# Kernel optimization log

Measured on AMD Instinct MI355X. Metric: run time of the kernel, lower is better.

## Reference

```python
import jax, jax.numpy as jnp
import numpy as np

N_HEADS = 16
ATT_DIM = 1024
HEAD_DIM = ATT_DIM // N_HEADS
SCALE = 1.0 / (HEAD_DIM ** 0.5)


def setup_inputs() -> dict:
    key = jax.random.key(0)
    k1, k2 = jax.random.split(key)
    B, N, D = 4, 2048, 1024
    X = jax.random.normal(k1, (B, N, D), dtype=jnp.float32)
    W_qkv = jax.random.normal(k2, (3 * ATT_DIM, D), dtype=jnp.float32) * 0.02  # trunc_normal-ish std
    return {"X": X, "W_qkv": W_qkv}


def reference(X, W_qkv):
    B, N, D = X.shape
    # qkv projection (bias=False): X @ W^T -> [b, n, 3*att_dim]
    QKV = jnp.einsum('bnd,od->bno', X, W_qkv)
    # rearrange 'b n (p h d) -> p b h n d'
    QKV = QKV.reshape(B, N, 3, N_HEADS, HEAD_DIM).transpose(2, 0, 3, 1, 4)
    Q, K, V = QKV[0], QKV[1], QKV[2]
    # scaled dot-product attention, full NxN scores (as in source)
    scores = jnp.einsum('bhid,bhjd->bhij', Q, K) * SCALE
    S = jax.nn.softmax(scores, axis=-1)
    # dropout rate is 0.0 -> identity
    Y = jnp.einsum('bhij,bhjd->bhid', S, V)
    # 'b h n d -> b n (h d)'; out_proj is Identity (out_dim == att_dim)
    return Y.transpose(0, 2, 1, 3).reshape(B, N, N_HEADS * HEAD_DIM)
```

## Files before the change

### kernel.cpp

```cpp
#include <hip/hip_runtime.h>

#define BATCH   4
#define SEQ     2048
#define DMODEL  1024
#define NHEADS  16
#define HDIM    64
#define QSC     0.18033688f

typedef short s16x8 __attribute__((ext_vector_type(8)));
typedef float f32x4 __attribute__((ext_vector_type(4)));
typedef const __attribute__((address_space(1))) unsigned int* gas_t;
typedef __attribute__((address_space(3))) unsigned int* las_t;

__device__ inline unsigned short f2bf(float f) {
    unsigned int u = __float_as_uint(f);
    u += 0x7FFF + ((u >> 16) & 1);
    return (unsigned short)(u >> 16);
}

__device__ __forceinline__ float exp2_fast(float x) {
#if __has_builtin(__builtin_amdgcn_exp2f)
    return __builtin_amdgcn_exp2f(x);
#else
    return exp2f(x);
#endif
}

__device__ __forceinline__ float rcp_fast(float x) {
#if __has_builtin(__builtin_amdgcn_rcpf)
    return __builtin_amdgcn_rcpf(x);
#else
    return 1.0f / x;
#endif
}

__device__ __forceinline__ unsigned int pack_bf16x2(float lo, float hi) {
    unsigned int a = __float_as_uint(lo) + 0x8000u;
    unsigned int b = __float_as_uint(hi) + 0x8000u;
#if __has_builtin(__builtin_amdgcn_perm)
    return __builtin_amdgcn_perm(b, a, 0x07060302u);
#else
    return (a >> 16) | (b & 0xFFFF0000u);
#endif
}

__global__ void cvt_bf16_2(const float* __restrict__ a,
                           unsigned short* __restrict__ oa, int n4a,
                           const float* __restrict__ bsrc,
                           unsigned short* __restrict__ ob, int n4b) {
    int i = blockIdx.x * blockDim.x + threadIdx.x;
    if (i < n4a) {
        float4 v = ((const float4*)a)[i];
        ushort4 o;
        o.x = f2bf(v.x); o.y = f2bf(v.y); o.z = f2bf(v.z); o.w = f2bf(v.w);
        ((ushort4*)oa)[i] = o;
    } else {
        int j = i - n4a;
        if (j < n4b) {
            float4 v = ((const float4*)bsrc)[j];
            ushort4 o;
            o.x = f2bf(v.x); o.y = f2bf(v.y); o.z = f2bf(v.z); o.w = f2bf(v.w);
            ((ushort4*)ob)[j] = o;
        }
    }
}

__global__ __launch_bounds__(256) void qkv_gemm(
    const unsigned short* __restrict__ Xb,
    const unsigned short* __restrict__ Wb,
    unsigned short* __restrict__ Qo,
    unsigned short* __restrict__ Ko,
    unsigned short* __restrict__ Vt)
{
    __shared__ __align__(16) unsigned short As[2 * 128 * 32];
    __shared__ __align__(16) unsigned short Bs[2 * 128 * 32];

    const int t    = threadIdx.x;
    const int flat = blockIdx.y * 24 + blockIdx.x;
    const int sw   = (flat & 7) * 192 + (flat >> 3);
    const int m0   = (sw / 24) * 128;
    const int n0   = (sw % 24) * 128;

    const int wid  = t >> 6;
    const int lane = t & 63;
    const int l15  = lane & 15;
    const int quad = lane >> 4;
    const int wm   = (wid >> 1) * 64;
    const int wn   = (wid & 1) * 64;

    const int rA   = wid * 32 + (lane >> 2);
    const int kcol_phys = (lane & 3) * 8;
    const int kcol_src  = ((lane & 3) ^ ((rA >> 1) & 3)) * 8;
    const unsigned short* gA = &Xb[(size_t)(m0 + rA) * 1024 + kcol_src];
    const unsigned short* gB = &Wb[(size_t)(n0 + rA) * 1024 + kcol_src];

    const int cswq = (quad ^ ((l15 >> 1) & 3)) * 8;

    f32x4 acc[4][4] = {};

    auto stage = [&](int k0, int bufE) {
        #pragma unroll
        for (int rd = 0; rd < 2; rd++) {
            __builtin_amdgcn_global_load_lds(
                (gas_t)(const void*)(gA + rd * 16 * 1024 + k0),
                (las_t)(void*)&As[bufE + (rA + rd * 16) * 32 + kcol_phys], 16, 0, 0);
            __builtin_amdgcn_global_load_lds(
                (gas_t)(const void*)(gB + rd * 16 * 1024 + k0),
                (las_t)(void*)&Bs[bufE + (rA + rd * 16) * 32 + kcol_phys], 16, 0, 0);
        }
    };

    auto comp = [&](int bufE) {
        s16x8 af[4], bf[4];
        #pragma unroll
        for (int mt = 0; mt < 4; mt++)
            af[mt] = *(const s16x8*)&As[bufE + (wm + mt * 16 + l15) * 32 + cswq];
        #pragma unroll
        for (int nt = 0; nt < 4; nt++)
            bf[nt] = *(const s16x8*)&Bs[bufE + (wn + nt * 16 + l15) * 32 + cswq];
        #pragma unroll
        for (int mt = 0; mt < 4; mt++)
            #pragma unroll
            for (int nt = 0; nt < 4; nt++)
                acc[mt][nt] = __builtin_amdgcn_mfma_f32_16x16x32_bf16(
                    af[mt], bf[nt], acc[mt][nt], 0, 0, 0);
    };

    stage(0, 0);
    __syncthreads();

    #pragma unroll 1
    for (int k0 = 0; k0 < 1024; k0 += 64) {
        stage(k0 + 32, 4096);
        comp(0);
        __syncthreads();
        if (k0 + 64 < 1024) stage(k0 + 64, 0);
        comp(4096);
        __syncthreads();
    }

    #pragma unroll
    for (int mt = 0; mt < 4; mt++) {
        const int mbase = m0 + wm + mt * 16 + quad * 4;
        const int b     = mbase >> 11;
        const int nbase = mbase & 2047;
        #pragma unroll
        for (int nt = 0; nt < 4; nt++) {
            const int o  = n0 + wn + nt * 16 + l15;
            const int p  = o >> 10;
            const int oo = o & 1023;
            const int h  = oo >> 6;
            const int d  = oo & 63;
            if (p == 0) {
                #pragma unroll
                for (int r = 0; r < 4; r++)
                    Qo[((size_t)(b * 16 + h) * 2048 + nbase + r) * 64 + d] =
                        f2bf(acc[mt][nt][r] * QSC);
            } else if (p == 1) {
                #pragma unroll
                for (int r = 0; r < 4; r++)
                    Ko[((size_t)(b * 16 + h) * 2048 + nbase + r) * 64 + d] =
                        f2bf(acc[mt][nt][r]);
            } else {
                ushort4 v4;
                v4.x = f2bf(acc[mt][nt][0]);
                v4.y = f2bf(acc[mt][nt][1]);
                v4.z = f2bf(acc[mt][nt][2]);
                v4.w = f2bf(acc[mt][nt][3]);
                *(ushort4*)&Vt[((size_t)(b * 16 + h) * 64 + d) * 2048 + nbase] = v4;
            }
        }
    }
}

#define PSTRIDE 72
#define PBASE   16384

__global__ __launch_bounds__(512) void attn(
    const unsigned short* __restrict__ Q,
    const unsigned short* __restrict__ K,
    const unsigned short* __restrict__ Vt,
    float* __restrict__ out)
{
    __shared__ __align__(16) unsigned short LDS[PBASE + 8 * 32 * PSTRIDE];

    const int t    = threadIdx.x;
    const int w    = t >> 6;
    const int lane = t & 63;
    const int l15  = lane & 15;
    const int quad = lane >> 4;
    const int head = blockIdx.y;
    const int b    = head >> 4;
    const int h    = head & 15;
    const int q0   = blockIdx.x * 256 + w * 32;

    const unsigned short* Qh = Q  + (size_t)head * 2048 * 64;
    const unsigned short* Kh = K  + (size_t)head * 2048 * 64;
    const unsigned short* Vh = Vt + (size_t)head * 64 * 2048;

    const int r0 = t >> 3;
    const int c0 = (t & 7) ^ (r0 & 7);
    const unsigned short* srcK = Kh + r0 * 64 + c0 * 8;
    const unsigned short* srcV = Vh + r0 * 2048 + c0 * 8;

    auto stageKV = [&](int kt, int bufE) {
        __builtin_amdgcn_global_load_lds(
            (gas_t)(const void*)(srcK + kt * 4096),
            (las_t)(void*)&LDS[bufE + t * 8], 16, 0, 0);
        __builtin_amdgcn_global_load_lds(
            (gas_t)(const void*)(srcV + kt * 64),
            (las_t)(void*)&LDS[bufE + 4096 + t * 8], 16, 0, 0);
    };

    s16x8 qb[2][2];
    #pragma unroll
    for (int mt = 0; mt < 2; mt++)
        #pragma unroll
        for (int kc = 0; kc < 2; kc++)
            qb[mt][kc] = *(const s16x8*)&Qh[(size_t)(q0 + mt * 16 + l15) * 64 + kc * 32 + quad * 8];

    s16x8 onesf;
    #pragma unroll
    for (int i = 0; i < 8; i++) onesf[i] = (short)0x3F80;
    const f32x4 fz = {0.f, 0.f, 0.f, 0.f};

    f32x4 y[2][4] = {};
    f32x4 ysum[2] = {};
    unsigned short* P = &LDS[PBASE + w * (32 * PSTRIDE)];

    const int x7   = l15 & 7;
    const int csw0 = (quad ^ x7) * 8;
    const int csw1 = ((4 + quad) ^ x7) * 8;

    auto compute = [&](int bufE) {
        s16x8 kb[4][2];
        #pragma unroll
        for (int nt = 0; nt < 4; nt++) {
            const int rowb = bufE + (nt * 16 + l15) * 64;
            kb[nt][0] = *(const s16x8*)&LDS[rowb + csw0];
            kb[nt][1] = *(const s16x8*)&LDS[rowb + csw1];
        }
        f32x4 st[4][2];
        #pragma unroll
        for (int nt = 0; nt < 4; nt++)
            #pragma unroll
            for (int mt = 0; mt < 2; mt++)
                st[nt][mt] = __builtin_amdgcn_mfma_f32_16x16x32_bf16(
                    kb[nt][0], qb[mt][0], fz, 0, 0, 0);
        #pragma unroll
        for (int nt = 0; nt < 4; nt++)
            #pragma unroll
            for (int mt = 0; mt < 2; mt++)
                st[nt][mt] = __builtin_amdgcn_mfma_f32_16x16x32_bf16(
                    kb[nt][1], qb[mt][1], st[nt][mt], 0, 0, 0);
        s16x8 vb[4][2];
        #pragma unroll
        for (int dt = 0; dt < 4; dt++) {
            const int rowb = bufE + 4096 + (dt * 16 + l15) * 64;
            vb[dt][0] = *(const s16x8*)&LDS[rowb + csw0];
            vb[dt][1] = *(const s16x8*)&LDS[rowb + csw1];
        }
        #pragma unroll
        for (int mt = 0; mt < 2; mt++)
            #pragma unroll
            for (int nt = 0; nt < 4; nt++) {
                float p0 = exp2_fast(st[nt][mt][0]);
                float p1 = exp2_fast(st[nt][mt][1]);
                float p2 = exp2_fast(st[nt][mt][2]);
                float p3 = exp2_fast(st[nt][mt][3]);
                uint2 u;
                u.x = pack_bf16x2(p0, p1);
                u.y = pack_bf16x2(p2, p3);
                *(uint2*)&P[(mt * 16 + l15) * PSTRIDE + nt * 16 + quad * 4] = u;
            }
        #pragma unroll
        for (int kc = 0; kc < 2; kc++) {
            s16x8 pa[2];
            #pragma unroll
            for (int mt = 0; mt < 2; mt++)
                pa[mt] = *(const s16x8*)&P[(mt * 16 + l15) * PSTRIDE + kc * 32 + quad * 8];
            #pragma unroll
            for (int mt = 0; mt < 2; mt++)
                ysum[mt] = __builtin_amdgcn_mfma_f32_16x16x32_bf16(
                    pa[mt], onesf, ysum[mt], 0, 0, 0);
            #pragma unroll
            for (int mt = 0; mt < 2; mt++)
                #pragma unroll
                for (int dt = 0; dt < 4; dt++)
                    y[mt][dt] = __builtin_amdgcn_mfma_f32_16x16x32_bf16(
                        pa[mt], vb[dt][kc], y[mt][dt], 0, 0, 0);
        }
    };

    stageKV(0, 0);
    __syncthreads();

    #pragma unroll 1
    for (int kt = 0; kt < 32; kt += 2) {
        stageKV(kt + 1, 8192);
        compute(0);
        __syncthreads();
        if (kt + 2 < 32) stageKV(kt + 2, 0);
        compute(8192);
        __syncthreads();
    }

    float rinv[2][4];
    #pragma unroll
    for (int mt = 0; mt < 2; mt++)
        #pragma unroll
        for (int r = 0; r < 4; r++)
            rinv[mt][r] = rcp_fast(ysum[mt][r]);

    #pragma unroll
    for (int mt = 0; mt < 2; mt++)
        #pragma unroll
        for (int dt = 0; dt < 4; dt++)
            #pragma unroll
            for (int r = 0; r < 4; r++) {
                const int n = q0 + mt * 16 + quad * 4 + r;
                const int d = dt * 16 + l15;
                out[((size_t)(b * 2048 + n)) * 1024 + h * 64 + d] =
                    y[mt][dt][r] * rinv[mt][r];
            }
}

extern "C" void kernel_launch(void* const* d_in, const int* in_sizes, int n_in,
                              void* d_out, int out_size, void* d_ws, size_t ws_size,
                              hipStream_t stream) {
    const float* X = (const float*)d_in[0];
    const float* W = (const float*)d_in[1];
    float* out = (float*)d_out;

    char* ws = (char*)d_ws;
    unsigned short* Xb = (unsigned short*)(ws);
    unsigned short* Wb = (unsigned short*)(ws + 16777216);
    unsigned short* Qb = (unsigned short*)(ws + 23068672);
    unsigned short* Kb = (unsigned short*)(ws + 39845888);
    unsigned short* Vt = (unsigned short*)(ws + 56623104);

    cvt_bf16_2<<<dim3(11264), dim3(256), 0, stream>>>(X, Xb, 2097152, W, Wb, 786432);
    qkv_gemm<<<dim3(24, 64), dim3(256), 0, stream>>>(Xb, Wb, Qb, Kb, Vt);
    attn<<<dim3(8, 64), dim3(512), 0, stream>>>(Qb, Kb, Vt, out);
}
```

Before: 243.6 us.

## Retile QKV GEMM to 256x192 blocks with 8 waves and split-phase pipelining

The QKV projection GEMM moves from 128x128 tiles with 4 waves to 256x192 tiles with 8 waves. Each wave now computes a 128x48 sub-tile. The k-loop is split into two half-phases that interleave LDS fragment reads, async global-to-LDS staging of the next A and B tiles, and MFMA bursts. The bursts are bracketed by s_setprio and raw barriers. This aims to raise arithmetic intensity per LDS byte and overlap loads with compute, at the cost of more registers per thread and fewer blocks in flight.

```diff
diff --git a/kernel.cpp b/kernel.cpp
--- a/kernel.cpp
+++ b/kernel.cpp
@@ -65,88 +65,118 @@
     }
 }
 
-__global__ __launch_bounds__(256) void qkv_gemm(
+__global__ __launch_bounds__(512) void qkv_gemm(
     const unsigned short* __restrict__ Xb,
     const unsigned short* __restrict__ Wb,
     unsigned short* __restrict__ Qo,
     unsigned short* __restrict__ Ko,
     unsigned short* __restrict__ Vt)
 {
-    __shared__ __align__(16) unsigned short As[2 * 128 * 32];
-    __shared__ __align__(16) unsigned short Bs[2 * 128 * 32];
+    __shared__ __align__(16) unsigned short As[2 * 8192];
+    __shared__ __align__(16) unsigned short Bs[2 * 6144];
 
     const int t    = threadIdx.x;
-    const int flat = blockIdx.y * 24 + blockIdx.x;
-    const int sw   = (flat & 7) * 192 + (flat >> 3);
-    const int m0   = (sw / 24) * 128;
-    const int n0   = (sw % 24) * 128;
+    const int flat = blockIdx.y * 16 + blockIdx.x;
+    const int sw   = (flat & 7) * 64 + (flat >> 3);
+    const int m0   = (sw >> 4) * 256;
+    const int n0   = (sw & 15) * 192;
 
     const int wid  = t >> 6;
     const int lane = t & 63;
     const int l15  = lane & 15;
     const int quad = lane >> 4;
-    const int wm   = (wid >> 1) * 64;
-    const int wn   = (wid & 1) * 64;
-
-    const int rA   = wid * 32 + (lane >> 2);
-    const int kcol_phys = (lane & 3) * 8;
-    const int kcol_src  = ((lane & 3) ^ ((rA >> 1) & 3)) * 8;
-    const unsigned short* gA = &Xb[(size_t)(m0 + rA) * 1024 + kcol_src];
-    const unsigned short* gB = &Wb[(size_t)(n0 + rA) * 1024 + kcol_src];
+    const int wr   = wid >> 2;
+    const int wc   = wid & 3;
+
+    const int srow = t >> 2;
+    const int csrc = ((t & 3) ^ ((t >> 3) & 3)) * 8;
+    const unsigned short* gA = &Xb[(size_t)(m0 + srow) * 1024 + csrc];
+    const unsigned short* gB = &Wb[(size_t)(n0 + srow) * 1024 + csrc];
 
     const int cswq = (quad ^ ((l15 >> 1) & 3)) * 8;
 
-    f32x4 acc[4][4] = {};
-
-    auto stage = [&](int k0, int bufE) {
-        #pragma unroll
-        for (int rd = 0; rd < 2; rd++) {
+    const int arow = wr * 128 + l15;
+    const int brow = wc * 48 + l15;
+
+    f32x4 acc[8][3] = {};
+
+    auto stageA = [&](int k0, int bufE) {
+        #pragma unroll
+        for (int g = 0; g < 2; g++)
             __builtin_amdgcn_global_load_lds(
-                (gas_t)(const void*)(gA + rd * 16 * 1024 + k0),
-                (las_t)(void*)&As[bufE + (rA + rd * 16) * 32 + kcol_phys], 16, 0, 0);
+                (gas_t)(const void*)(gA + (size_t)g * 131072 + k0),
+                (las_t)(void*)&As[bufE + (g * 512 + t) * 8], 16, 0, 0);
+    };
+    auto stageB = [&](int k0, int bufE) {
+        __builtin_amdgcn_global_load_lds(
+            (gas_t)(const void*)(gB + k0),
+            (las_t)(void*)&Bs[bufE + t * 8], 16, 0, 0);
+        if (wid < 4)
             __builtin_amdgcn_global_load_lds(
-                (gas_t)(const void*)(gB + rd * 16 * 1024 + k0),
-                (las_t)(void*)&Bs[bufE + (rA + rd * 16) * 32 + kcol_phys], 16, 0, 0);
-        }
+                (gas_t)(const void*)(gB + (size_t)131072 + k0),
+                (las_t)(void*)&Bs[bufE + (512 + t) * 8], 16, 0, 0);
     };
 
-    auto comp = [&](int bufE) {
-        s16x8 af[4], bf[4];
-        #pragma unroll
-        for (int mt = 0; mt < 4; mt++)
-            af[mt] = *(const s16x8*)&As[bufE + (wm + mt * 16 + l15) * 32 + cswq];
-        #pragma unroll
-        for (int nt = 0; nt < 4; nt++)
-            bf[nt] = *(const s16x8*)&Bs[bufE + (wn + nt * 16 + l15) * 32 + cswq];
-        #pragma unroll
-        for (int mt = 0; mt < 4; mt++)
-            #pragma unroll
-            for (int nt = 0; nt < 4; nt++)
-                acc[mt][nt] = __builtin_amdgcn_mfma_f32_16x16x32_bf16(
-                    af[mt], bf[nt], acc[mt][nt], 0, 0, 0);
-    };
-
-    stage(0, 0);
+    stageA(0, 0);
+    stageB(0, 0);
     __syncthreads();
 
     #pragma unroll 1
-    for (int k0 = 0; k0 < 1024; k0 += 64) {
-        stage(k0 + 32, 4096);
-        comp(0);
-        __syncthreads();
-        if (k0 + 64 < 1024) stage(k0 + 64, 0);
-        comp(4096);
-        __syncthreads();
+    for (int T = 0; T < 32; T++) {
+        const int bufA = (T & 1) * 8192;
+        const int bufB = (T & 1) * 6144;
+        const int oA   = 8192 - bufA;
+        const int oB   = 6144 - bufB;
+        const int kn   = (T + 1) * 32;
+
+        s16x8 bfr[3];
+        {
+            s16x8 afr[4];
+            #pragma unroll
+            for (int mr = 0; mr < 4; mr++)
+                afr[mr] = *(const s16x8*)&As[bufA + (arow + mr * 16) * 32 + cswq];
+            #pragma unroll
+            for (int nr = 0; nr < 3; nr++)
+                bfr[nr] = *(const s16x8*)&Bs[bufB + (brow + nr * 16) * 32 + cswq];
+            if (T < 31) stageA(kn, oA);
+            __builtin_amdgcn_s_barrier();
+            __builtin_amdgcn_s_setprio(1);
+            #pragma unroll
+            for (int mr = 0; mr < 4; mr++)
+                #pragma unroll
+                for (int nr = 0; nr < 3; nr++)
+                    acc[mr][nr] = __builtin_amdgcn_mfma_f32_16x16x32_bf16(
+                        afr[mr], bfr[nr], acc[mr][nr], 0, 0, 0);
+            __builtin_amdgcn_s_setprio(0);
+            __builtin_amdgcn_s_barrier();
+        }
+        {
+            s16x8 afr[4];
+            #pragma unroll
+            for (int mr = 0; mr < 4; mr++)
+                afr[mr] = *(const s16x8*)&As[bufA + (arow + (4 + mr) * 16) * 32 + cswq];
+            if (T < 31) stageB(kn, oB);
+            __builtin_amdgcn_s_barrier();
+            __builtin_amdgcn_s_setprio(1);
+            #pragma unroll
+            for (int mr = 0; mr < 4; mr++)
+                #pragma unroll
+                for (int nr = 0; nr < 3; nr++)
+                    acc[4 + mr][nr] = __builtin_amdgcn_mfma_f32_16x16x32_bf16(
+                        afr[mr], bfr[nr], acc[4 + mr][nr], 0, 0, 0);
+            __builtin_amdgcn_s_setprio(0);
+            __syncthreads();
+        }
     }
 
     #pragma unroll
-    for (int mt = 0; mt < 4; mt++) {
-        const int mbase = m0 + wm + mt * 16 + quad * 4;
+    for (int mrep = 0; mrep < 8; mrep++) {
+        const int mbase = m0 + wr * 128 + mrep * 16 + quad * 4;
         const int b     = mbase >> 11;
         const int nbase = mbase & 2047;
         #pragma unroll
-        for (int nt = 0; nt < 4; nt++) {
-            const int o  = n0 + wn + nt * 16 + l15;
+        for (int nrep = 0; nrep < 3; nrep++) {
+            const int o  = n0 + wc * 48 + nrep * 16 + l15;
             const int p  = o >> 10;
             const int oo = o & 1023;
             const int h  = oo >> 6;
@@ -155,18 +185,18 @@
                 #pragma unroll
                 for (int r = 0; r < 4; r++)
                     Qo[((size_t)(b * 16 + h) * 2048 + nbase + r) * 64 + d] =
-                        f2bf(acc[mt][nt][r] * QSC);
+                        f2bf(acc[mrep][nrep][r] * QSC);
             } else if (p == 1) {
                 #pragma unroll
                 for (int r = 0; r < 4; r++)
                     Ko[((size_t)(b * 16 + h) * 2048 + nbase + r) * 64 + d] =
-                        f2bf(acc[mt][nt][r]);
+                        f2bf(acc[mrep][nrep][r]);
             } else {
                 ushort4 v4;
-                v4.x = f2bf(acc[mt][nt][0]);
-                v4.y = f2bf(acc[mt][nt][1]);
-                v4.z = f2bf(acc[mt][nt][2]);
-                v4.w = f2bf(acc[mt][nt][3]);
+                v4.x = f2bf(acc[mrep][nrep][0]);
+                v4.y = f2bf(acc[mrep][nrep][1]);
+                v4.z = f2bf(acc[mrep][nrep][2]);
+                v4.w = f2bf(acc[mrep][nrep][3]);
                 *(ushort4*)&Vt[((size_t)(b * 16 + h) * 64 + d) * 2048 + nbase] = v4;
             }
         }
@@ -340,6 +370,6 @@
     unsigned short* Vt = (unsigned short*)(ws + 56623104);
 
     cvt_bf16_2<<<dim3(11264), dim3(256), 0, stream>>>(X, Xb, 2097152, W, Wb, 786432);
-    qkv_gemm<<<dim3(24, 64), dim3(256), 0, stream>>>(Xb, Wb, Qb, Kb, Vt);
+    qkv_gemm<<<dim3(16, 32), dim3(512), 0, stream>>>(Xb, Wb, Qb, Kb, Vt);
     attn<<<dim3(8, 64), dim3(512), 0, stream>>>(Qb, Kb, Vt, out);
 }
```

Result: faster. 227.2 us (-6.7%).
